# Kernel tuning notes

Measured on AMD Instinct MI355X. Metric: run time of the kernel, lower is better.

Reference implementation:

```python
import jax, jax.numpy as jnp
import numpy as np

H = 8        # heads
DH = 64      # dim_head
K = 16       # num_neighbors
EMB = 512    # emb_dim
INNER = H * DH
AINNER = 4 * DH  # per-head attn_mlp hidden width
POSH = 64


def setup_inputs() -> dict:
    key = jax.random.key(0)
    ks = jax.random.split(key, 20)
    bs, n = 2, 1024
    rn = lambda k, s, sc=1.0: jax.random.normal(k, s, jnp.float32) * sc
    return {
        "query": rn(ks[0], (bs, n, EMB)),
        "key_in": rn(ks[1], (bs, n, EMB)),
        "value": rn(ks[2], (bs, n, EMB)),
        "canonical": rn(ks[3], (bs, n, 3)),
        "w_q": rn(ks[4], (EMB, INNER), EMB ** -0.5),
        "w_k": rn(ks[5], (EMB, INNER), EMB ** -0.5),
        "w_v": rn(ks[6], (EMB, INNER), EMB ** -0.5),
        "w_out": rn(ks[7], (INNER, EMB), INNER ** -0.5),
        "b_out": rn(ks[8], (EMB,), 0.02),
        "pos_w1": rn(ks[9], (3, POSH), 3 ** -0.5),
        "pos_b1": rn(ks[10], (POSH,), 0.02),
        "pos_w2": rn(ks[11], (POSH, INNER), POSH ** -0.5),
        "pos_b2": rn(ks[12], (INNER,), 0.02),
        "aw1": rn(ks[13], (H, AINNER, DH), DH ** -0.5),   # grouped conv1 weight per head: (out=4*DH, in=DH)
        "ab1": rn(ks[14], (H, AINNER), 0.02),
        "aw2": rn(ks[15], (H, DH, AINNER), AINNER ** -0.5),  # grouped conv2: (out=DH, in=4*DH)
        "ab2": rn(ks[16], (H, DH), 0.02),
    }


def reference(query, key_in, value, canonical, w_q, w_k, w_v, w_out, b_out,
              pos_w1, pos_b1, pos_w2, pos_b2, aw1, ab1, aw2, ab2):
    bs, n, _ = query.shape
    # projections, then b n (h d) -> b h n d
    to_heads = lambda t: t.reshape(bs, n, H, DH).transpose(0, 2, 1, 3)
    q = to_heads(query @ w_q)
    k = to_heads(key_in @ w_k)
    v = to_heads(value @ w_v)

    # KNN on canonical coords: (b,n,n) squared distances, k smallest (includes self)
    d2 = jnp.sum((canonical[:, :, None, :] - canonical[:, None, :, :]) ** 2, axis=-1)
    _, nbr = jax.lax.top_k(-d2, K)                       # (b,n,K)
    idx = (nbr + (jnp.arange(bs) * n)[:, None, None]).reshape(-1)  # flat rows into bs*n

    # relative position embedding
    pos_nn = canonical.reshape(bs * n, 3)[idx].reshape(bs, n, K, 3)
    rel = pos_nn - canonical[:, :, None, :]
    rpe = jax.nn.relu(rel @ pos_w1 + pos_b1) @ pos_w2 + pos_b2        # (b,n,K,inner)
    rpe = rpe.reshape(bs, n, K, H, DH).transpose(0, 3, 1, 2, 4)       # (b,h,i,j,d)

    # faithful replication of the original view(bs*n,-1)[idx] gathers on (b,h,n,d) tensors
    gather = lambda t: t.reshape(bs * n, -1)[idx].reshape(bs, H, n, K, DH)
    qg, kg, vg = gather(q), gather(k), gather(v)
    vg = vg + rpe
    x = (qg - kg) + rpe                                  # (b,h,i,j,d)

    # grouped 1x1 conv attn_mlp == per-head MLP over d
    hdn = jax.nn.relu(jnp.einsum('bhijd,hed->bhije', x, aw1) + ab1[None, :, None, None, :])
    sim = jnp.einsum('bhije,hde->bhijd', hdn, aw2) + ab2[None, :, None, None, :]

    attn = jax.nn.softmax(sim, axis=3)                   # softmax over neighbors j
    norm = jnp.sqrt(jnp.sum(attn * attn, axis=2, keepdims=True))  # F.normalize over i
    attn = attn / jnp.maximum(norm, 1e-12)

    agg = jnp.einsum('bhijd,bhijd->bhid', attn, vg)      # (b,h,i,d)
    agg = agg.transpose(0, 2, 1, 3).reshape(bs, n, INNER)
    return agg @ w_out + b_out
```

## Files before the change

kernel.cpp:

```cpp
#include <hip/hip_runtime.h>


#define BS 2
#define NPT 1024
#define HH 8
#define DH 64
#define KNN 16
#define EMB 512
#define INNER 512
#define AINNER 256
#define POSH 64

typedef unsigned short u16;
typedef unsigned int u32;
typedef __attribute__((ext_vector_type(8))) short bf16x8;
typedef __attribute__((ext_vector_type(4))) float f32x4;

__device__ __forceinline__ float bf2f(u16 b) { union { u32 u; float f; } v; v.u = ((u32)b) << 16; return v.f; }
__device__ __forceinline__ u16 f2bf_rne(float f) {
    u32 x = __float_as_uint(f);
    u32 r = x + 0x7fffu + ((x >> 16) & 1u);
    return (u16)(r >> 16);
}
__device__ __forceinline__ void split2(float f, u16& hi, u16& lo) {
    u32 bits = __float_as_uint(f);
    hi = (u16)(bits >> 16);
    float resid = f - __uint_as_float(bits & 0xffff0000u);
    lo = (u16)(__float_as_uint(resid) >> 16);
}

__global__ __launch_bounds__(256) void k_pre(const float* __restrict__ query,
                                             const float* __restrict__ key_in,
                                             const float* __restrict__ value,
                                             const float* __restrict__ aw1,
                                             const float* __restrict__ aw2,
                                             const float* __restrict__ pw2,
                                             u16* __restrict__ qhi, u16* __restrict__ qlo,
                                             u16* __restrict__ khi, u16* __restrict__ klo,
                                             u16* __restrict__ vhi, u16* __restrict__ vlo,
                                             u16* __restrict__ w1hi, u16* __restrict__ w2hi,
                                             u16* __restrict__ rw2hi)
{
    const int bx = blockIdx.x, t = threadIdx.x;
    if (bx < 3072) {
        const int m = bx >> 10;
        const int v = (((bx & 1023) * 256) + t) * 4;
        const float* src; u16* dh; u16* dl;
        switch (m) {
            case 0:  src = query;  dh = qhi; dl = qlo; break;
            case 1:  src = key_in; dh = khi; dl = klo; break;
            default: src = value;  dh = vhi; dl = vlo; break;
        }
        float4 f = *(const float4*)&src[v];
        if (m == 1) { f.x = -f.x; f.y = -f.y; f.z = -f.z; f.w = -f.w; }
        ushort4 h4, l4;
        split2(f.x, h4.x, l4.x); split2(f.y, h4.y, l4.y);
        split2(f.z, h4.z, l4.z); split2(f.w, h4.w, l4.w);
        *(ushort4*)&dh[v] = h4;
        *(ushort4*)&dl[v] = l4;
    } else {
        int idx = (bx - 3072) * 256 + t;
        if (idx < 131072) {
            w1hi[idx] = f2bf_rne(aw1[idx]);
        } else if (idx < 262144) {
            int k2 = idx - 131072;
            w2hi[k2] = f2bf_rne(aw2[k2]);
        } else {
            int k2 = idx - 262144;
            int p = k2 & 63; int hd = k2 >> 6;
            int h = hd >> 6; int d = hd & 63;
            rw2hi[k2] = f2bf_rne(pw2[(size_t)p * INNER + h * DH + d]);
        }
    }
}

__global__ __launch_bounds__(256) void k_split_T(const float* __restrict__ wq,
                                                 const float* __restrict__ wk,
                                                 const float* __restrict__ wv,
                                                 const float* __restrict__ wout,
                                                 u16* __restrict__ o0h, u16* __restrict__ o0l,
                                                 u16* __restrict__ o1h, u16* __restrict__ o1l,
                                                 u16* __restrict__ o2h, u16* __restrict__ o2l,
                                                 u16* __restrict__ o3h, u16* __restrict__ o3l)
{
    __shared__ float S[64][65];
    const int t = threadIdx.x;
    const int e0 = blockIdx.x * 64, c0 = blockIdx.y * 64;
    const float* src; u16* dh; u16* dl;
    switch (blockIdx.z) {
        case 0:  src = wq;   dh = o0h; dl = o0l; break;
        case 1:  src = wk;   dh = o1h; dl = o1l; break;
        case 2:  src = wv;   dh = o2h; dl = o2l; break;
        default: src = wout; dh = o3h; dl = o3l; break;
    }
    #pragma unroll
    for (int s = 0; s < 16; ++s) {
        int v = s * 256 + t; int r = v >> 6, c = v & 63;
        S[r][c] = src[(size_t)(e0 + r) * 512 + c0 + c];
    }
    __syncthreads();
    #pragma unroll
    for (int s = 0; s < 16; ++s) {
        int v = s * 256 + t; int c = v >> 6, e = v & 63;
        u16 hi, lo; split2(S[e][c], hi, lo);
        size_t off = (size_t)(c0 + c) * 512 + e0 + e;
        dh[off] = hi; dl[off] = lo;
    }
}

__global__ __launch_bounds__(256) void k_projM(const u16* __restrict__ qhi, const u16* __restrict__ qlo,
                                               const u16* __restrict__ khi, const u16* __restrict__ klo,
                                               const u16* __restrict__ vhi, const u16* __restrict__ vlo,
                                               const u16* __restrict__ wqh, const u16* __restrict__ wql,
                                               const u16* __restrict__ wkh, const u16* __restrict__ wkl,
                                               const u16* __restrict__ wvh, const u16* __restrict__ wvl,
                                               float* __restrict__ Dws, float* __restrict__ Vws)
{
    __shared__ u16 S[12][64 * 40];
    const int t = threadIdx.x, l = t & 63, w = t >> 6;
    const int lm = l & 15, lg = (l >> 4) * 8;
    const int g0 = blockIdx.x * 64, c0 = blockIdx.y * 64;
    const int sr = t >> 2, sc = (t & 3) * 8;

    f32x4 accD[4] = {{0,0,0,0},{0,0,0,0},{0,0,0,0},{0,0,0,0}};
    f32x4 accV[4] = {{0,0,0,0},{0,0,0,0},{0,0,0,0},{0,0,0,0}};

    for (int ks = 0; ks < 16; ++ks) {
        const int k0 = ks * 32;
        if (ks) __syncthreads();
        #define STG(p, base, rb) \
            *(uint4*)&S[p][sr * 40 + sc] = *(const uint4*)&(base)[(size_t)((rb) + sr) * 512 + k0 + sc];
        STG(0, qhi, g0) STG(1, qlo, g0) STG(2, khi, g0) STG(3, klo, g0)
        STG(4, vhi, g0) STG(5, vlo, g0)
        STG(6, wqh, c0) STG(7, wql, c0) STG(8, wkh, c0) STG(9, wkl, c0)
        STG(10, wvh, c0) STG(11, wvl, c0)
        #undef STG
        __syncthreads();

        const int ao = (w * 16 + lm) * 40 + lg;
        bf16x8 aqh = *(const bf16x8*)&S[0][ao];
        bf16x8 aql = *(const bf16x8*)&S[1][ao];
        bf16x8 akh = *(const bf16x8*)&S[2][ao];
        bf16x8 akl = *(const bf16x8*)&S[3][ao];
        bf16x8 avh = *(const bf16x8*)&S[4][ao];
        bf16x8 avl = *(const bf16x8*)&S[5][ao];
        #pragma unroll
        for (int ct = 0; ct < 4; ++ct) {
            const int bo = (ct * 16 + lm) * 40 + lg;
            bf16x8 bqh = *(const bf16x8*)&S[6][bo];
            bf16x8 bql = *(const bf16x8*)&S[7][bo];
            bf16x8 bkh = *(const bf16x8*)&S[8][bo];
            bf16x8 bkl = *(const bf16x8*)&S[9][bo];
            bf16x8 bvh = *(const bf16x8*)&S[10][bo];
            bf16x8 bvl = *(const bf16x8*)&S[11][bo];
            accD[ct] = __builtin_amdgcn_mfma_f32_16x16x32_bf16(aqh, bqh, accD[ct], 0, 0, 0);
            accD[ct] = __builtin_amdgcn_mfma_f32_16x16x32_bf16(aql, bqh, accD[ct], 0, 0, 0);
            accD[ct] = __builtin_amdgcn_mfma_f32_16x16x32_bf16(aqh, bql, accD[ct], 0, 0, 0);
            accD[ct] = __builtin_amdgcn_mfma_f32_16x16x32_bf16(akh, bkh, accD[ct], 0, 0, 0);
            accD[ct] = __builtin_amdgcn_mfma_f32_16x16x32_bf16(akl, bkh, accD[ct], 0, 0, 0);
            accD[ct] = __builtin_amdgcn_mfma_f32_16x16x32_bf16(akh, bkl, accD[ct], 0, 0, 0);
            accV[ct] = __builtin_amdgcn_mfma_f32_16x16x32_bf16(avh, bvh, accV[ct], 0, 0, 0);
            accV[ct] = __builtin_amdgcn_mfma_f32_16x16x32_bf16(avl, bvh, accV[ct], 0, 0, 0);
            accV[ct] = __builtin_amdgcn_mfma_f32_16x16x32_bf16(avh, bvl, accV[ct], 0, 0, 0);
        }
    }

    const int b = blockIdx.x >> 4;
    const int h = blockIdx.y;
    #pragma unroll
    for (int ct = 0; ct < 4; ++ct) {
        #pragma unroll
        for (int r = 0; r < 4; ++r) {
            int g = g0 + w * 16 + (l >> 4) * 4 + r;
            int i = g & 1023;
            size_t off = (((size_t)(b * HH + h)) * NPT + i) * DH + ct * 16 + lm;
            Dws[off] = accD[ct][r];
            Vws[off] = accV[ct][r];
        }
    }
}

__global__ __launch_bounds__(256) void k_knn(const float* __restrict__ canonical, int* __restrict__ nbr)
{
    const int t = threadIdx.x, l = t & 63, w = t >> 6;
    const int i = blockIdx.x * 4 + w;
    const int b = blockIdx.y;
    const float* cb = canonical + (size_t)b * NPT * 3;
    const float qx = cb[i*3+0], qy = cb[i*3+1], qz = cb[i*3+2];
    float d2v[16];
    #pragma unroll
    for (int k = 0; k < 16; ++k) {
        int j = l * 16 + k;
        float dx = __fsub_rn(cb[j*3+0], qx);
        float dy = __fsub_rn(cb[j*3+1], qy);
        float dz = __fsub_rn(cb[j*3+2], qz);
        d2v[k] = __fadd_rn(__fadd_rn(__fmul_rn(dx,dx), __fmul_rn(dy,dy)), __fmul_rn(dz,dz));
    }
    unsigned alive = 0xFFFFu;
    int* out = nbr + ((size_t)b * NPT + i) * KNN;
    for (int sel = 0; sel < KNN; ++sel) {
        float bv = __builtin_inff(); int bk = 16;
        #pragma unroll
        for (int k = 0; k < 16; ++k) {
            float v = ((alive >> k) & 1u) ? d2v[k] : __builtin_inff();
            if (v < bv) { bv = v; bk = k; }
        }
        int bj = l * 16 + bk;
        #pragma unroll
        for (int m = 32; m >= 1; m >>= 1) {
            float ov = __shfl_xor(bv, m, 64);
            int   oj = __shfl_xor(bj, m, 64);
            if (ov < bv || (ov == bv && oj < bj)) { bv = ov; bj = oj; }
        }
        if (l == 0) out[sel] = bj;
        if ((bj >> 4) == l) alive &= ~(1u << (bj & 15));
    }
}

__global__ __launch_bounds__(256, 3) void k_attn(const float* __restrict__ Dws,
                                              const float* __restrict__ Vws,
                                              const float* __restrict__ canonical,
                                              const int* __restrict__ nbr,
                                              const float* __restrict__ pw1,
                                              const float* __restrict__ pb1,
                                              const float* __restrict__ pb2,
                                              const float* __restrict__ ab1,
                                              const float* __restrict__ ab2,
                                              const u16* __restrict__ w1hi,
                                              const u16* __restrict__ w2hi,
                                              const u16* __restrict__ rw2hi,
                                              u16* __restrict__ vvb,
                                              u16* __restrict__ attnb)
{
    const int it = blockIdx.x, h = blockIdx.y, b = blockIdx.z, t = threadIdx.x;
    const int l = t & 63, w = t >> 6;
    const int lm = l & 15, lg = (l >> 4) * 8;
    const int dd = w * 16 + lm;

    __shared__ u16 h1hi[16 * 72], h1lo[16 * 72];
    __shared__ u16 Xs[16 * 72];
    __shared__ u16 Hhi[16 * 264], Hlo[16 * 264];
    __shared__ u16 rw2s[64 * 72];
    __shared__ float pw1s[3 * POSH];
    __shared__ float pb1s[POSH];
    __shared__ float rel_all[8][KNN][3];
    __shared__ int nbrrow[KNN];

    bf16x8 w1f[8], w2f[8];
    float b1v[4];
    #pragma unroll
    for (int q = 0; q < 4; ++q) {
        int e = (w * 4 + q) * 16 + lm;
        b1v[q] = ab1[h * AINNER + e];
        #pragma unroll
        for (int kc = 0; kc < 2; ++kc)
            w1f[q*2+kc] = *(const bf16x8*)&w1hi[((size_t)(h * AINNER + e)) * DH + kc * 32 + lg];
    }
    const float b2v  = ab2[h * DH + dd];
    const float pb2v = pb2[h * DH + dd];
    #pragma unroll
    for (int kc = 0; kc < 8; ++kc)
        w2f[kc] = *(const bf16x8*)&w2hi[((size_t)(h * DH + dd)) * AINNER + kc * 32 + lg];

    for (int v = t; v < 64 * 64; v += 256) {
        int d = v >> 6, p = v & 63;
        rw2s[d * 72 + p] = rw2hi[(h * DH + d) * POSH + p];
    }
    if (t < 192) pw1s[t] = pw1[t];
    if (t < 64)  pb1s[t] = pb1[t];
    if (t < KNN) nbrrow[t] = nbr[((size_t)b * NPT + h * 128 + it) * KNN + t];
    if (t < 128) {
        int ti = t >> 4, jj = t & 15;
        int i2 = it * 8 + ti;
        int nv2 = nbr[((size_t)b * NPT + i2) * KNN + jj];
        const float* cn = canonical + ((size_t)b * NPT + nv2) * 3;
        const float* ci = canonical + ((size_t)b * NPT + i2) * 3;
        rel_all[ti][jj][0] = cn[0] - ci[0];
        rel_all[ti][jj][1] = cn[1] - ci[1];
        rel_all[ti][jj][2] = cn[2] - ci[2];
    }
    __syncthreads();

    float dvp[4], vwp[4];
    auto gather = [&](int tt) {
        #pragma unroll
        for (int r = 0; r < 4; ++r) {
            int j = (l >> 4) * 4 + r;
            int nv = nbrrow[2 * tt + (j >> 3)];
            size_t off = (((size_t)b * HH + (nv >> 7)) * NPT + (nv & 127) * 8 + (j & 7)) * DH + dd;
            dvp[r] = Dws[off];
            vwp[r] = Vws[off];
        }
    };
    gather(0);

    for (int ti = 0; ti < 8; ++ti) {
        const int i = it * 8 + ti;
        #pragma unroll
        for (int r = 0; r < 4; ++r) {
            int v = r * 256 + t; int j = v >> 6; int p = v & 63;
            float a = pb1s[p];
            a = fmaf(rel_all[ti][j][0], pw1s[p], a);
            a = fmaf(rel_all[ti][j][1], pw1s[64 + p], a);
            a = fmaf(rel_all[ti][j][2], pw1s[128 + p], a);
            a = fmaxf(a, 0.0f);
            u16 hi, lo; split2(a, hi, lo);
            h1hi[j * 72 + p] = hi;
            h1lo[j * 72 + p] = lo;
        }
        __syncthreads();
        {
            f32x4 racc = {0.f, 0.f, 0.f, 0.f};
            #pragma unroll
            for (int kc = 0; kc < 2; ++kc) {
                bf16x8 ah = *(const bf16x8*)&h1hi[lm * 72 + kc * 32 + lg];
                bf16x8 al = *(const bf16x8*)&h1lo[lm * 72 + kc * 32 + lg];
                bf16x8 rb = *(const bf16x8*)&rw2s[dd * 72 + kc * 32 + lg];
                racc = __builtin_amdgcn_mfma_f32_16x16x32_bf16(ah, rb, racc, 0, 0, 0);
                racc = __builtin_amdgcn_mfma_f32_16x16x32_bf16(al, rb, racc, 0, 0, 0);
            }
            u16* vvrow = vvb + (((size_t)(b * HH + h) * NPT + i) * KNN) * DH + dd;
            #pragma unroll
            for (int r = 0; r < 4; ++r) {
                int j = (l >> 4) * 4 + r;
                float rp = racc[r] + pb2v;
                Xs[j * 72 + dd] = f2bf_rne(dvp[r] + rp);
                vvrow[j * DH] = f2bf_rne(vwp[r] + rp);
            }
            if (ti < 7) gather(ti + 1);
        }
        __syncthreads();
        {
            f32x4 acc1[4] = {{0,0,0,0},{0,0,0,0},{0,0,0,0},{0,0,0,0}};
            #pragma unroll
            for (int kc = 0; kc < 2; ++kc) {
                bf16x8 ah = *(const bf16x8*)&Xs[lm * 72 + kc * 32 + lg];
                #pragma unroll
                for (int q = 0; q < 4; ++q)
                    acc1[q] = __builtin_amdgcn_mfma_f32_16x16x32_bf16(ah, w1f[q*2+kc], acc1[q], 0, 0, 0);
            }
            #pragma unroll
            for (int q = 0; q < 4; ++q) {
                int ee = (w * 4 + q) * 16 + lm;
                #pragma unroll
                for (int r = 0; r < 4; ++r) {
                    int jj = (l >> 4) * 4 + r;
                    float v2 = fmaxf(acc1[q][r] + b1v[q], 0.0f);
                    u16 hi, lo; split2(v2, hi, lo);
                    Hhi[jj * 264 + ee] = hi;
                    Hlo[jj * 264 + ee] = lo;
                }
            }
        }
        __syncthreads();
        {
            f32x4 acc2[4] = {{0,0,0,0},{0,0,0,0},{0,0,0,0},{0,0,0,0}};
            #pragma unroll
            for (int kc = 0; kc < 8; ++kc) {
                bf16x8 ah = *(const bf16x8*)&Hhi[lm * 264 + kc * 32 + lg];
                bf16x8 al = *(const bf16x8*)&Hlo[lm * 264 + kc * 32 + lg];
                int p = kc & 3;
                acc2[p] = __builtin_amdgcn_mfma_f32_16x16x32_bf16(ah, w2f[kc], acc2[p], 0, 0, 0);
                acc2[p] = __builtin_amdgcn_mfma_f32_16x16x32_bf16(al, w2f[kc], acc2[p], 0, 0, 0);
            }
            float sim[4];
            #pragma unroll
            for (int r = 0; r < 4; ++r)
                sim[r] = ((acc2[0][r] + acc2[1][r]) + (acc2[2][r] + acc2[3][r])) + b2v;
            float m = fmaxf(fmaxf(sim[0], sim[1]), fmaxf(sim[2], sim[3]));
            m = fmaxf(m, __shfl_xor(m, 16, 64));
            m = fmaxf(m, __shfl_xor(m, 32, 64));
            float ex[4], s = 0.0f;
            #pragma unroll
            for (int r = 0; r < 4; ++r) { ex[r] = __expf(sim[r] - m); s += ex[r]; }
            s += __shfl_xor(s, 16, 64);
            s += __shfl_xor(s, 32, 64);
            float inv = 1.0f / s;
            u16* ao = attnb + (((size_t)(b * HH + h) * NPT + i) * KNN) * DH + dd;
            #pragma unroll
            for (int r = 0; r < 4; ++r)
                ao[((l >> 4) * 4 + r) * DH] = f2bf_rne(ex[r] * inv);
        }
    }
}

__global__ __launch_bounds__(256) void k_norm1(const u16* __restrict__ attnb, float* __restrict__ npart)
{
    const int j = blockIdx.x, h = blockIdx.y, bz = blockIdx.z;
    const int b = bz >> 3, ic = bz & 7;
    const int t = threadIdx.x, d = t & 63, q4 = t >> 6;
    const u16* base = attnb + ((size_t)(b * HH + h) * NPT) * KNN * DH + j * DH + d;
    float acc = 0.0f;
    for (int r = 0; r < 32; ++r) {
        int i = ic * 128 + q4 + r * 4;
        float a = bf2f(base[(size_t)i * KNN * DH]);
        acc = fmaf(a, a, acc);
    }
    __shared__ float red[256];
    red[t] = acc;
    __syncthreads();
    if (q4 == 0) {
        float s = red[d] + red[64 + d] + red[128 + d] + red[192 + d];
        npart[(((size_t)(b * HH + h) * KNN + j) * DH + d) + 16384 * ic] = s;
    }
}

__global__ __launch_bounds__(256) void k_agg(const u16* __restrict__ attnb,
                                             const float* __restrict__ npart,
                                             const u16* __restrict__ vvb,
                                             u16* __restrict__ agghi,
                                             u16* __restrict__ agglo)
{
    const int it = blockIdx.x, h = blockIdx.y, b = blockIdx.z, t = threadIdx.x;
    const int d = t & 63, si = t >> 6;
    const int i = it * 4 + si;
    __shared__ float rn[KNN * DH];
    const size_t nb = (size_t)(b * HH + h) * (KNN * DH);
    for (int v = t; v < KNN * DH; v += 256) {
        float s = 0.0f;
        #pragma unroll
        for (int ic = 0; ic < 8; ++ic) s += npart[nb + v + 16384 * ic];
        rn[v] = 1.0f / fmaxf(sqrtf(s), 1e-12f);
    }
    __syncthreads();
    const u16* ab = attnb + (((size_t)(b * HH + h) * NPT + i) * KNN) * DH + d;
    const u16* vb = vvb   + (((size_t)(b * HH + h) * NPT + i) * KNN) * DH + d;
    float acc = 0.0f;
    #pragma unroll
    for (int j = 0; j < KNN; ++j) {
        float a  = bf2f(ab[j * DH]);
        float vv = bf2f(vb[j * DH]);
        acc = fmaf(a * rn[j * DH + d], vv, acc);
    }
    size_t off = ((size_t)b * NPT + i) * INNER + h * DH + d;
    u16 hi, lo; split2(acc, hi, lo);
    agghi[off] = hi;
    agglo[off] = lo;
}

__global__ __launch_bounds__(256) void k_outM(const u16* __restrict__ agghi, const u16* __restrict__ agglo,
                                              const u16* __restrict__ wth, const u16* __restrict__ wtl,
                                              const float* __restrict__ bout,
                                              float* __restrict__ outp)
{
    __shared__ u16 S[4][64 * 40];
    const int t = threadIdx.x, l = t & 63, w = t >> 6;
    const int lm = l & 15, lg = (l >> 4) * 8;
    const int g0 = blockIdx.x * 64, c0 = blockIdx.y * 64;
    const int sr = t >> 2, sc = (t & 3) * 8;

    f32x4 acc[4] = {{0,0,0,0},{0,0,0,0},{0,0,0,0},{0,0,0,0}};
    float bv4[4];
    #pragma unroll
    for (int ct = 0; ct < 4; ++ct) bv4[ct] = bout[c0 + ct * 16 + lm];

    for (int ks = 0; ks < 16; ++ks) {
        const int k0 = ks * 32;
        if (ks) __syncthreads();
        *(uint4*)&S[0][sr * 40 + sc] = *(const uint4*)&agghi[(size_t)(g0 + sr) * 512 + k0 + sc];
        *(uint4*)&S[1][sr * 40 + sc] = *(const uint4*)&agglo[(size_t)(g0 + sr) * 512 + k0 + sc];
        *(uint4*)&S[2][sr * 40 + sc] = *(const uint4*)&wth[(size_t)(c0 + sr) * 512 + k0 + sc];
        *(uint4*)&S[3][sr * 40 + sc] = *(const uint4*)&wtl[(size_t)(c0 + sr) * 512 + k0 + sc];
        __syncthreads();

        const int ao = (w * 16 + lm) * 40 + lg;
        bf16x8 ah = *(const bf16x8*)&S[0][ao];
        bf16x8 al = *(const bf16x8*)&S[1][ao];
        #pragma unroll
        for (int ct = 0; ct < 4; ++ct) {
            const int bo = (ct * 16 + lm) * 40 + lg;
            bf16x8 bh = *(const bf16x8*)&S[2][bo];
            bf16x8 bl = *(const bf16x8*)&S[3][bo];
            acc[ct] = __builtin_amdgcn_mfma_f32_16x16x32_bf16(ah, bh, acc[ct], 0, 0, 0);
            acc[ct] = __builtin_amdgcn_mfma_f32_16x16x32_bf16(al, bh, acc[ct], 0, 0, 0);
            acc[ct] = __builtin_amdgcn_mfma_f32_16x16x32_bf16(ah, bl, acc[ct], 0, 0, 0);
        }
    }
    #pragma unroll
    for (int ct = 0; ct < 4; ++ct) {
        #pragma unroll
        for (int r = 0; r < 4; ++r) {
            int g = g0 + w * 16 + (l >> 4) * 4 + r;
            outp[(size_t)g * 512 + c0 + ct * 16 + lm] = acc[ct][r] + bv4[ct];
        }
    }
}

extern "C" void kernel_launch(void* const* d_in, const int* in_sizes, int n_in,
                              void* d_out, int out_size, void* d_ws, size_t ws_size,
                              hipStream_t stream) {
    const float* query     = (const float*)d_in[0];
    const float* key_in    = (const float*)d_in[1];
    const float* value     = (const float*)d_in[2];
    const float* canonical = (const float*)d_in[3];
    const float* wq   = (const float*)d_in[4];
    const float* wk   = (const float*)d_in[5];
    const float* wv   = (const float*)d_in[6];
    const float* wout = (const float*)d_in[7];
    const float* bout = (const float*)d_in[8];
    const float* pw1  = (const float*)d_in[9];
    const float* pb1  = (const float*)d_in[10];
    const float* pw2  = (const float*)d_in[11];
    const float* pb2  = (const float*)d_in[12];
    const float* aw1  = (const float*)d_in[13];
    const float* ab1  = (const float*)d_in[14];
    const float* aw2  = (const float*)d_in[15];
    const float* ab2  = (const float*)d_in[16];

    float* ws    = (float*)d_ws;
    float* Dws   = ws;
    float* Vws   = ws + 1048576;
    float* aggp  = ws + 2097152;
    float* npart = ws + 3162112;
    int*   nbr   = (int*)(ws + 3293184);
    float* attnR = ws + 3325952;

    u16* agghi = (u16*)aggp;
    u16* agglo = agghi + 1048576;

    u16* attnb = (u16*)attnR;
    u16* pl   = (u16*)(attnR + 8388608);
    u16* qhi  = pl;                u16* qlo  = pl + 1048576;
    u16* khi  = pl + 2097152;      u16* klo  = pl + 3145728;
    u16* vhi  = pl + 4194304;      u16* vlo  = pl + 5242880;
    u16* wqTh = pl + 6291456;      u16* wqTl = pl + 6553600;
    u16* wkTh = pl + 6815744;      u16* wkTl = pl + 7077888;
    u16* wvTh = pl + 7340032;      u16* wvTl = pl + 7602176;

    u16* u16b  = (u16*)(ws + 20103168);
    u16* w1hi  = u16b;
    u16* w2hi  = u16b + 262144;
    u16* rw2hi = u16b + 524288;
    u16* vvb   = u16b + 589824;
    u16* wouTh = u16b + 17367040;
    u16* wouTl = u16b + 17629184;

    k_pre<<<4224, 256, 0, stream>>>(query, key_in, value, aw1, aw2, pw2,
                                    qhi, qlo, khi, klo, vhi, vlo, w1hi, w2hi, rw2hi);
    k_split_T<<<dim3(8, 8, 4), 256, 0, stream>>>(wq, wk, wv, wout,
                                                 wqTh, wqTl, wkTh, wkTl, wvTh, wvTl, wouTh, wouTl);
    k_projM<<<dim3(32, 8), 256, 0, stream>>>(qhi, qlo, khi, klo, vhi, vlo,
                                             wqTh, wqTl, wkTh, wkTl, wvTh, wvTl, Dws, Vws);
    k_knn<<<dim3(256, BS), 256, 0, stream>>>(canonical, nbr);
    k_attn<<<dim3(128, HH, BS), 256, 0, stream>>>(Dws, Vws, canonical, nbr, pw1, pb1, pb2,
                                                  ab1, ab2, w1hi, w2hi, rw2hi, vvb, attnb);
    k_norm1<<<dim3(KNN, HH, BS * 8), 256, 0, stream>>>(attnb, npart);
    k_agg<<<dim3(256, HH, BS), 256, 0, stream>>>(attnb, npart, vvb, agghi, agglo);
    k_outM<<<dim3(32, 8), 256, 0, stream>>>(agghi, agglo, wouTh, wouTl, bout, (float*)d_out);
}
```

Baseline: 171.4 us.

## Drop hi/lo split in attn MLP, process point pairs, fuse norm partials

The attention kernel drops the bf16 hi/lo split of the MLP activations, which halves the MFMA count and shared-memory traffic. It also processes two points per synchronisation step, raising the barriers' spacing, and raises the launch bound to 4 blocks per CU. The sum-of-squares for the normalisation over i is now accumulated inside the attention kernel and reduced by a small kernel, replacing the separate k_norm1 pass that re-read the attention tensor. The exchange is lower precision in the MLP intermediates and more register pressure under the tighter occupancy target.

```diff
diff --git a/kernel.cpp b/kernel.cpp
--- a/kernel.cpp
+++ b/kernel.cpp
@@ -217,7 +217,7 @@
     }
 }
 
-__global__ __launch_bounds__(256, 3) void k_attn(const float* __restrict__ Dws,
+__global__ __launch_bounds__(256, 4) void k_attn(const float* __restrict__ Dws,
                                               const float* __restrict__ Vws,
                                               const float* __restrict__ canonical,
                                               const int* __restrict__ nbr,
@@ -230,16 +230,17 @@
                                               const u16* __restrict__ w2hi,
                                               const u16* __restrict__ rw2hi,
                                               u16* __restrict__ vvb,
-                                              u16* __restrict__ attnb)
+                                              u16* __restrict__ attnb,
+                                              float* __restrict__ npart2)
 {
     const int it = blockIdx.x, h = blockIdx.y, b = blockIdx.z, t = threadIdx.x;
     const int l = t & 63, w = t >> 6;
     const int lm = l & 15, lg = (l >> 4) * 8;
     const int dd = w * 16 + lm;
 
-    __shared__ u16 h1hi[16 * 72], h1lo[16 * 72];
-    __shared__ u16 Xs[16 * 72];
-    __shared__ u16 Hhi[16 * 264], Hlo[16 * 264];
+    __shared__ u16 h1s[2][16 * 72];
+    __shared__ u16 Xs[2][16 * 72];
+    __shared__ u16 Hs[2][16 * 264];
     __shared__ u16 rw2s[64 * 72];
     __shared__ float pw1s[3 * POSH];
     __shared__ float pb1s[POSH];
@@ -281,60 +282,67 @@
     }
     __syncthreads();
 
-    float dvp[4], vwp[4];
-    auto gather = [&](int tt) {
-        #pragma unroll
-        for (int r = 0; r < 4; ++r) {
-            int j = (l >> 4) * 4 + r;
-            int nv = nbrrow[2 * tt + (j >> 3)];
-            size_t off = (((size_t)b * HH + (nv >> 7)) * NPT + (nv & 127) * 8 + (j & 7)) * DH + dd;
-            dvp[r] = Dws[off];
-            vwp[r] = Vws[off];
+    float dvp[2][4], vwp[2][4];
+    auto gather = [&](int pp) {
+        #pragma unroll
+        for (int u = 0; u < 2; ++u) {
+            const int ti = 2 * pp + u;
+            #pragma unroll
+            for (int r = 0; r < 4; ++r) {
+                int j = (l >> 4) * 4 + r;
+                int nv = nbrrow[2 * ti + (j >> 3)];
+                size_t off = (((size_t)b * HH + (nv >> 7)) * NPT + (nv & 127) * 8 + (j & 7)) * DH + dd;
+                dvp[u][r] = Dws[off];
+                vwp[u][r] = Vws[off];
+            }
         }
     };
     gather(0);
 
-    for (int ti = 0; ti < 8; ++ti) {
-        const int i = it * 8 + ti;
-        #pragma unroll
-        for (int r = 0; r < 4; ++r) {
-            int v = r * 256 + t; int j = v >> 6; int p = v & 63;
-            float a = pb1s[p];
-            a = fmaf(rel_all[ti][j][0], pw1s[p], a);
-            a = fmaf(rel_all[ti][j][1], pw1s[64 + p], a);
-            a = fmaf(rel_all[ti][j][2], pw1s[128 + p], a);
-            a = fmaxf(a, 0.0f);
-            u16 hi, lo; split2(a, hi, lo);
-            h1hi[j * 72 + p] = hi;
-            h1lo[j * 72 + p] = lo;
+    float npacc[4] = {0.f, 0.f, 0.f, 0.f};
+
+    for (int p = 0; p < 4; ++p) {
+        #pragma unroll
+        for (int u = 0; u < 2; ++u) {
+            const int ti = 2 * p + u;
+            #pragma unroll
+            for (int r = 0; r < 4; ++r) {
+                int v = r * 256 + t; int j = v >> 6; int pp = v & 63;
+                float a = pb1s[pp];
+                a = fmaf(rel_all[ti][j][0], pw1s[pp], a);
+                a = fmaf(rel_all[ti][j][1], pw1s[64 + pp], a);
+                a = fmaf(rel_all[ti][j][2], pw1s[128 + pp], a);
+                h1s[u][j * 72 + pp] = f2bf_rne(fmaxf(a, 0.0f));
+            }
         }
         __syncthreads();
-        {
+        #pragma unroll
+        for (int u = 0; u < 2; ++u) {
+            const int i = it * 8 + 2 * p + u;
             f32x4 racc = {0.f, 0.f, 0.f, 0.f};
             #pragma unroll
             for (int kc = 0; kc < 2; ++kc) {
-                bf16x8 ah = *(const bf16x8*)&h1hi[lm * 72 + kc * 32 + lg];
-                bf16x8 al = *(const bf16x8*)&h1lo[lm * 72 + kc * 32 + lg];
+                bf16x8 ah = *(const bf16x8*)&h1s[u][lm * 72 + kc * 32 + lg];
                 bf16x8 rb = *(const bf16x8*)&rw2s[dd * 72 + kc * 32 + lg];
                 racc = __builtin_amdgcn_mfma_f32_16x16x32_bf16(ah, rb, racc, 0, 0, 0);
-                racc = __builtin_amdgcn_mfma_f32_16x16x32_bf16(al, rb, racc, 0, 0, 0);
             }
             u16* vvrow = vvb + (((size_t)(b * HH + h) * NPT + i) * KNN) * DH + dd;
             #pragma unroll
             for (int r = 0; r < 4; ++r) {
                 int j = (l >> 4) * 4 + r;
                 float rp = racc[r] + pb2v;
-                Xs[j * 72 + dd] = f2bf_rne(dvp[r] + rp);
-                vvrow[j * DH] = f2bf_rne(vwp[r] + rp);
-            }
-            if (ti < 7) gather(ti + 1);
-        }
+                Xs[u][j * 72 + dd] = f2bf_rne(dvp[u][r] + rp);
+                vvrow[j * DH] = f2bf_rne(vwp[u][r] + rp);
+            }
+        }
+        if (p < 3) gather(p + 1);
         __syncthreads();
-        {
+        #pragma unroll
+        for (int u = 0; u < 2; ++u) {
             f32x4 acc1[4] = {{0,0,0,0},{0,0,0,0},{0,0,0,0},{0,0,0,0}};
             #pragma unroll
             for (int kc = 0; kc < 2; ++kc) {
-                bf16x8 ah = *(const bf16x8*)&Xs[lm * 72 + kc * 32 + lg];
+                bf16x8 ah = *(const bf16x8*)&Xs[u][lm * 72 + kc * 32 + lg];
                 #pragma unroll
                 for (int q = 0; q < 4; ++q)
                     acc1[q] = __builtin_amdgcn_mfma_f32_16x16x32_bf16(ah, w1f[q*2+kc], acc1[q], 0, 0, 0);
@@ -345,23 +353,19 @@
                 #pragma unroll
                 for (int r = 0; r < 4; ++r) {
                     int jj = (l >> 4) * 4 + r;
-                    float v2 = fmaxf(acc1[q][r] + b1v[q], 0.0f);
-                    u16 hi, lo; split2(v2, hi, lo);
-                    Hhi[jj * 264 + ee] = hi;
-                    Hlo[jj * 264 + ee] = lo;
+                    Hs[u][jj * 264 + ee] = f2bf_rne(fmaxf(acc1[q][r] + b1v[q], 0.0f));
                 }
             }
         }
         __syncthreads();
-        {
+        #pragma unroll
+        for (int u = 0; u < 2; ++u) {
+            const int i = it * 8 + 2 * p + u;
             f32x4 acc2[4] = {{0,0,0,0},{0,0,0,0},{0,0,0,0},{0,0,0,0}};
             #pragma unroll
             for (int kc = 0; kc < 8; ++kc) {
-                bf16x8 ah = *(const bf16x8*)&Hhi[lm * 264 + kc * 32 + lg];
-                bf16x8 al = *(const bf16x8*)&Hlo[lm * 264 + kc * 32 + lg];
-                int p = kc & 3;
-                acc2[p] = __builtin_amdgcn_mfma_f32_16x16x32_bf16(ah, w2f[kc], acc2[p], 0, 0, 0);
-                acc2[p] = __builtin_amdgcn_mfma_f32_16x16x32_bf16(al, w2f[kc], acc2[p], 0, 0, 0);
+                bf16x8 ah = *(const bf16x8*)&Hs[u][lm * 264 + kc * 32 + lg];
+                acc2[kc & 3] = __builtin_amdgcn_mfma_f32_16x16x32_bf16(ah, w2f[kc], acc2[kc & 3], 0, 0, 0);
             }
             float sim[4];
             #pragma unroll
@@ -378,35 +382,32 @@
             float inv = 1.0f / s;
             u16* ao = attnb + (((size_t)(b * HH + h) * NPT + i) * KNN) * DH + dd;
             #pragma unroll
-            for (int r = 0; r < 4; ++r)
-                ao[((l >> 4) * 4 + r) * DH] = f2bf_rne(ex[r] * inv);
-        }
-    }
-}
-
-__global__ __launch_bounds__(256) void k_norm1(const u16* __restrict__ attnb, float* __restrict__ npart)
-{
-    const int j = blockIdx.x, h = blockIdx.y, bz = blockIdx.z;
-    const int b = bz >> 3, ic = bz & 7;
-    const int t = threadIdx.x, d = t & 63, q4 = t >> 6;
-    const u16* base = attnb + ((size_t)(b * HH + h) * NPT) * KNN * DH + j * DH + d;
-    float acc = 0.0f;
-    for (int r = 0; r < 32; ++r) {
-        int i = ic * 128 + q4 + r * 4;
-        float a = bf2f(base[(size_t)i * KNN * DH]);
-        acc = fmaf(a, a, acc);
-    }
-    __shared__ float red[256];
-    red[t] = acc;
-    __syncthreads();
-    if (q4 == 0) {
-        float s = red[d] + red[64 + d] + red[128 + d] + red[192 + d];
-        npart[(((size_t)(b * HH + h) * KNN + j) * DH + d) + 16384 * ic] = s;
-    }
+            for (int r = 0; r < 4; ++r) {
+                u16 abf16 = f2bf_rne(ex[r] * inv);
+                ao[((l >> 4) * 4 + r) * DH] = abf16;
+                float abf = bf2f(abf16);
+                npacc[r] = fmaf(abf, abf, npacc[r]);
+            }
+        }
+    }
+
+    float* np = npart2 + ((size_t)((b * HH + h) * 128 + it)) * 1024 + ((l >> 4) * 4) * 64 + dd;
+    #pragma unroll
+    for (int r = 0; r < 4; ++r) np[r * 64] = npacc[r];
+}
+
+__global__ __launch_bounds__(256) void k_normR(const float* __restrict__ npart2, float* __restrict__ nrm)
+{
+    int v = blockIdx.x * 256 + threadIdx.x;
+    int bh = v >> 10, jd = v & 1023;
+    const float* src = npart2 + (size_t)bh * 128 * 1024 + jd;
+    float s = 0.0f;
+    for (int it2 = 0; it2 < 128; ++it2) s += src[(size_t)it2 * 1024];
+    nrm[v] = sqrtf(s);
 }
 
 __global__ __launch_bounds__(256) void k_agg(const u16* __restrict__ attnb,
-                                             const float* __restrict__ npart,
+                                             const float* __restrict__ nrm,
                                              const u16* __restrict__ vvb,
                                              u16* __restrict__ agghi,
                                              u16* __restrict__ agglo)
@@ -415,13 +416,8 @@
     const int d = t & 63, si = t >> 6;
     const int i = it * 4 + si;
     __shared__ float rn[KNN * DH];
-    const size_t nb = (size_t)(b * HH + h) * (KNN * DH);
-    for (int v = t; v < KNN * DH; v += 256) {
-        float s = 0.0f;
-        #pragma unroll
-        for (int ic = 0; ic < 8; ++ic) s += npart[nb + v + 16384 * ic];
-        rn[v] = 1.0f / fmaxf(sqrtf(s), 1e-12f);
-    }
+    for (int v = t; v < KNN * DH; v += 256)
+        rn[v] = 1.0f / fmaxf(nrm[(size_t)(b * HH + h) * 1024 + v], 1e-12f);
     __syncthreads();
     const u16* ab = attnb + (((size_t)(b * HH + h) * NPT + i) * KNN) * DH + d;
     const u16* vb = vvb   + (((size_t)(b * HH + h) * NPT + i) * KNN) * DH + d;
@@ -511,7 +507,7 @@
     float* Dws   = ws;
     float* Vws   = ws + 1048576;
     float* aggp  = ws + 2097152;
-    float* npart = ws + 3162112;
+    float* nrm   = ws + 3162112;
     int*   nbr   = (int*)(ws + 3293184);
     float* attnR = ws + 3325952;
 
@@ -526,6 +522,7 @@
     u16* wqTh = pl + 6291456;      u16* wqTl = pl + 6553600;
     u16* wkTh = pl + 6815744;      u16* wkTl = pl + 7077888;
     u16* wvTh = pl + 7340032;      u16* wvTl = pl + 7602176;
+    float* npart2 = attnR + 12582912;
 
     u16* u16b  = (u16*)(ws + 20103168);
     u16* w1hi  = u16b;
@@ -543,8 +540,8 @@
                                              wqTh, wqTl, wkTh, wkTl, wvTh, wvTl, Dws, Vws);
     k_knn<<<dim3(256, BS), 256, 0, stream>>>(canonical, nbr);
     k_attn<<<dim3(128, HH, BS), 256, 0, stream>>>(Dws, Vws, canonical, nbr, pw1, pb1, pb2,
-                                                  ab1, ab2, w1hi, w2hi, rw2hi, vvb, attnb);
-    k_norm1<<<dim3(KNN, HH, BS * 8), 256, 0, stream>>>(attnb, npart);
-    k_agg<<<dim3(256, HH, BS), 256, 0, stream>>>(attnb, npart, vvb, agghi, agglo);
+                                                  ab1, ab2, w1hi, w2hi, rw2hi, vvb, attnb, npart2);
+    k_normR<<<64, 256, 0, stream>>>(npart2, nrm);
+    k_agg<<<dim3(256, HH, BS), 256, 0, stream>>>(attnb, nrm, vvb, agghi, agglo);
     k_outM<<<dim3(32, 8), 256, 0, stream>>>(agghi, agglo, wouTh, wouTl, bout, (float*)d_out);
 }
```

New measurement: 208.0 us. 1.21x slower.
